# Kernel tuning notes

Hardware: AMD Instinct MI355X
Metric: run time of the kernel (lower is better)

The kernel has to match this reference:

```python
import jax, jax.numpy as jnp
import numpy as np

D = 256
N_TOK, N_SRL, N_ENT, T = 50000, 20000, 10000, 50000
E_TS, E_EE, E_ST, E_ET = 300000, 150000, 300000, 150000
SLOPE = 0.01  # F.leaky_relu default negative slope


def _leaky(x):
    return jnp.where(x >= 0, x, SLOPE * x)


def _seg_softmax(e, seg, n):
    # per-destination (segment) softmax over incoming edges, elementwise per feature
    mx = jax.ops.segment_max(e, seg, num_segments=n)
    mx = jnp.where(jnp.isfinite(mx), mx, 0.0)
    ex = jnp.exp(e - mx[seg])
    den = jax.ops.segment_sum(ex, seg, num_segments=n)
    return ex / jnp.maximum(den[seg], 1e-9)


def _gru_cell(x, h, W_ih, W_hh, b_ih, b_hh):
    # PyTorch GRU cell: gates ordered (r, z, n)
    gi = x @ W_ih.T + b_ih
    gh = h @ W_hh.T + b_hh
    ir, iz, in_ = jnp.split(gi, 3, axis=-1)
    hr, hz, hn = jnp.split(gh, 3, axis=-1)
    r = jax.nn.sigmoid(ir + hr)
    z = jax.nn.sigmoid(iz + hz)
    n = jnp.tanh(in_ + r * hn)
    return (1.0 - z) * n + z * h


def _covering_dst(key, E, N):
    # every dst node gets >= 1 edge (matches DGL UDF-reduce update semantics)
    return jax.random.permutation(key, jnp.arange(E, dtype=jnp.int32) % N)


def setup_inputs():
    key = jax.random.key(0)
    ks = jax.random.split(key, 32)
    f32 = jnp.float32
    inp = {
        'feat_tok': jax.random.normal(ks[0], (N_TOK, D), f32),
        'feat_srl': jax.random.normal(ks[1], (N_SRL, D), f32),
        'feat_ent': jax.random.normal(ks[2], (N_ENT, D), f32),
        'bert_token_emb': jax.random.normal(ks[3], (T, D), f32),
        'rel_type': jax.random.uniform(ks[4], (E_EE,), f32),
        'src_ts': jax.random.randint(ks[5], (E_TS,), 0, N_TOK, jnp.int32),
        'dst_ts': _covering_dst(ks[6], E_TS, N_SRL),
        'src_ee': jax.random.randint(ks[7], (E_EE,), 0, N_ENT, jnp.int32),
        'dst_ee': _covering_dst(ks[8], E_EE, N_ENT),
        'src_st': jax.random.randint(ks[9], (E_ST,), 0, N_SRL, jnp.int32),
        'dst_st': _covering_dst(ks[10], E_ST, N_TOK),
        'src_et': jax.random.randint(ks[11], (E_ET,), 0, N_ENT, jnp.int32),
        'dst_et': _covering_dst(ks[12], E_ET, N_TOK),
    }
    x0 = jax.random.randint(ks[13], (E_EE,), 0, T - 64, jnp.int32)
    ln = jax.random.randint(ks[14], (E_EE,), 1, 65, jnp.int32)
    inp['span_idx'] = jnp.stack([x0, x0 + ln], axis=1)
    s = 0.05
    inp['W_node_trans'] = jax.random.normal(ks[15], (D, D), f32) * s
    inp['b_node_trans'] = jnp.zeros((D,), f32)
    inp['W_node_att'] = jax.random.normal(ks[16], (D, 2 * D), f32) * s
    inp['b_node_att'] = jnp.zeros((D,), f32)
    inp['W_rel_trans'] = jax.random.normal(ks[17], (D, 2 * D), f32) * s
    inp['b_rel_trans'] = jnp.zeros((D,), f32)
    inp['W_common'] = jax.random.normal(ks[18], (D, D), f32) * s
    inp['b_common'] = jnp.zeros((D,), f32)
    inp['W_ih'] = jax.random.normal(ks[19], (3 * D, D), f32) * s
    inp['W_hh'] = jax.random.normal(ks[20], (3 * D, D), f32) * s
    inp['b_ih'] = jax.random.normal(ks[21], (3 * D,), f32) * s
    inp['b_hh'] = jax.random.normal(ks[22], (3 * D,), f32) * s
    return inp


def reference(feat_tok, feat_srl, feat_ent, bert_token_emb, rel_type,
              W_node_trans, b_node_trans, W_node_att, b_node_att,
              W_rel_trans, b_rel_trans, W_common, b_common,
              W_ih, W_hh, b_ih, b_hh,
              src_ts, dst_ts, src_ee, dst_ee, span_idx,
              src_st, dst_st, src_et, dst_et):
    # ---- regular edges tok->srl (message_func_regular_node + reduce_func) ----
    us = feat_tok[src_ts] @ W_node_trans.T + b_node_trans          # [E_TS, D]
    ud = feat_srl[dst_ts] @ W_node_trans.T + b_node_trans
    e_ts = _leaky(jnp.concatenate([us, ud], axis=1) @ W_node_att.T + b_node_att)
    alpha_ts = _seg_softmax(e_ts, dst_ts, N_SRL)
    h_srl = jax.ops.segment_sum(alpha_ts * us, dst_ts, num_segments=N_SRL)

    # ---- ent2ent_rel (message_func_rel + reduce_func) ----
    # mean of bert_token_emb[x:y] via prefix sums (vectorized span means)
    P = jnp.concatenate([jnp.zeros((1, D), bert_token_emb.dtype),
                         jnp.cumsum(bert_token_emb, axis=0)], axis=0)  # [T+1, D]
    x, y = span_idx[:, 0], span_idx[:, 1]
    span_mean = (P[y] - P[x]) / (y - x).astype(P.dtype)[:, None]
    rel_emb = rel_type[:, None] * span_mean                         # [E_EE, D]
    src_e = feat_ent[src_ee]
    m_ee = (jnp.concatenate([src_e, rel_emb], axis=1) @ W_rel_trans.T + b_rel_trans)
    m_ee = m_ee @ W_common.T + b_common
    dst_p = feat_ent[dst_ee] @ W_node_trans.T + b_node_trans
    e_ee = _leaky(jnp.concatenate([m_ee, dst_p], axis=1) @ W_node_att.T + b_node_att)
    alpha_ee = _seg_softmax(e_ee, dst_ee, N_ENT)
    h_ent = jax.ops.segment_sum(alpha_ee * m_ee, dst_ee, num_segments=N_ENT)

    # ---- srl2tok / ent2tok: per-edge GRU step then segment-sum on tok ----
    m_st = _gru_cell(h_srl[src_st], feat_tok[dst_st], W_ih, W_hh, b_ih, b_hh)
    h_srl_tok = jax.ops.segment_sum(m_st, dst_st, num_segments=N_TOK)
    m_et = _gru_cell(h_ent[src_et], feat_tok[dst_et], W_ih, W_hh, b_ih, b_hh)
    h_ent_tok = jax.ops.segment_sum(m_et, dst_et, num_segments=N_TOK)

    # ---- final GRU combine: seq (h_ent_tok, feat_tok), hidden h_srl_tok ----
    h1 = _gru_cell(h_ent_tok, h_srl_tok, W_ih, W_hh, b_ih, b_hh)
    h_tok = _gru_cell(feat_tok, h1, W_ih, W_hh, b_ih, b_hh)

    return h_tok, h_srl, h_ent
```

## Files before the change

kernel.cpp:

```cpp
#include <hip/hip_runtime.h>
#include <stdint.h>


typedef unsigned short u16;
typedef __bf16 bf16_t;
typedef bf16_t bf16x8 __attribute__((ext_vector_type(8)));
typedef float f32x4 __attribute__((ext_vector_type(4)));

__device__ __forceinline__ float us2f(u16 h) {
  unsigned int u = ((unsigned int)h) << 16;
  return __builtin_bit_cast(float, u);
}
__device__ __forceinline__ u16 f2us(float f) {
  unsigned int u = __builtin_bit_cast(unsigned int, f);
  u += 0x7FFFu + ((u >> 16) & 1u);
  return (u16)(u >> 16);
}
__device__ __forceinline__ uint4 pack8(float4 a, float4 b) {
  uint4 v;
  v.x = f2us(a.x) | ((unsigned)f2us(a.y) << 16);
  v.y = f2us(a.z) | ((unsigned)f2us(a.w) << 16);
  v.z = f2us(b.x) | ((unsigned)f2us(b.y) << 16);
  v.w = f2us(b.z) | ((unsigned)f2us(b.w) << 16);
  return v;
}
__device__ __forceinline__ void us2f4(ushort4 v, float* o) {
  o[0] = us2f(v.x); o[1] = us2f(v.y); o[2] = us2f(v.z); o[3] = us2f(v.w);
}
__device__ __forceinline__ float sigm(float x) { return 1.f / (1.f + __expf(-x)); }
__device__ __forceinline__ float tanh_f(float x) {
  x = fminf(fmaxf(x, -15.f), 15.f);
  float e = __expf(2.f * x);
  return (e - 1.f) / (e + 1.f);
}

__global__ void fill_sent(float* out, int n, float v) {
  int i = blockIdx.x * 256 + threadIdx.x;
  if (i < n) out[i] = v;
}

__global__ void count_k(const int* __restrict__ dst, int E, int* __restrict__ cnt) {
  int i = blockIdx.x * 256 + threadIdx.x;
  if (i < E) atomicAdd(&cnt[dst[i]], 1);
}

__global__ __launch_bounds__(1024) void scan4_k(int* a0, int n0, int* a1, int n1,
                                                int* a2, int n2, int* a3, int n3) {
  int* a; int n;
  if (blockIdx.x == 0) { a = a0; n = n0; }
  else if (blockIdx.x == 1) { a = a1; n = n1; }
  else if (blockIdx.x == 2) { a = a2; n = n2; }
  else { a = a3; n = n3; }
  __shared__ int swv[16];
  const int t = threadIdx.x, lane = t & 63, wid = t >> 6;
  int carry = 0;
  for (int base = 0; base < n; base += 1024) {
    int r = base + t;
    int v = (r < n) ? a[r] : 0;
    int inc = v;
#pragma unroll
    for (int o = 1; o < 64; o <<= 1) {
      int x = __shfl_up(inc, o, 64);
      if (lane >= o) inc += x;
    }
    if (lane == 63) swv[wid] = inc;
    __syncthreads();
    int wbase = 0, tot = 0;
    for (int w = 0; w < 16; w++) { int s = swv[w]; tot += s; if (w < wid) wbase += s; }
    if (r < n) a[r] = carry + wbase + inc - v;
    carry += tot;
    __syncthreads();
  }
}

__global__ void fill_k(const int* __restrict__ dst, int E, int* __restrict__ off,
                       int* __restrict__ list) {
  int i = blockIdx.x * 256 + threadIdx.x;
  if (i < E) {
    int p = atomicAdd(&off[dst[i]], 1);
    list[p] = i;
  }
}

__global__ __launch_bounds__(256) void cumsum_p1(const float* __restrict__ emb,
                                                 float* __restrict__ bsum) {
  int b = blockIdx.x, t = threadIdx.x;
  int r0 = b * 64, r1 = min(r0 + 64, 50000);
  float acc = 0.f;
  for (int r = r0; r < r1; r++) acc += emb[(size_t)r * 256 + t];
  bsum[(size_t)b * 256 + t] = acc;
}
__global__ __launch_bounds__(256) void cumsum_p2p(float* __restrict__ bsum, int nb) {
  const int d = blockIdx.x;
  const int t = threadIdx.x, lane = t & 63, wid = t >> 6;
  __shared__ float wsum[4];
  float v[4];
  float s = 0.f;
#pragma unroll
  for (int j = 0; j < 4; j++) {
    int b = t * 4 + j;
    v[j] = (b < nb) ? bsum[(size_t)b * 256 + d] : 0.f;
    s += v[j];
  }
  float inc = s;
#pragma unroll
  for (int o = 1; o < 64; o <<= 1) {
    float x = __shfl_up(inc, o, 64);
    if (lane >= o) inc += x;
  }
  if (lane == 63) wsum[wid] = inc;
  __syncthreads();
  float wbase = 0.f;
  for (int w = 0; w < 4; w++) {
    float ws = wsum[w];
    if (w < wid) wbase += ws;
  }
  float excl = wbase + inc - s;
#pragma unroll
  for (int j = 0; j < 4; j++) {
    int b = t * 4 + j;
    if (b < nb) bsum[(size_t)b * 256 + d] = excl;
    excl += v[j];
  }
}
__global__ __launch_bounds__(256) void cumsum_p3(const float* __restrict__ emb,
                                                 const float* __restrict__ bsum,
                                                 float* __restrict__ Pm) {
  int b = blockIdx.x, t = threadIdx.x;
  int r0 = b * 64, r1 = min(r0 + 64, 50000);
  float acc = bsum[(size_t)b * 256 + t];
  if (b == 0) Pm[t] = 0.f;
  for (int r = r0; r < r1; r++) {
    acc += emb[(size_t)r * 256 + t];
    Pm[(size_t)(r + 1) * 256 + t] = acc;
  }
}

__global__ __launch_bounds__(256) void make_B2(const float* __restrict__ Watt,
                                               const float* __restrict__ Wc,
                                               float* __restrict__ B2) {
  int r = blockIdx.x, k = threadIdx.x;
  float s = 0.f;
  for (int n = 0; n < 256; n++) s += Watt[r * 512 + n] * Wc[n * 256 + k];
  B2[r * 256 + k] = s;
}
__global__ void make_bias2(const float* __restrict__ Watt, const float* __restrict__ bc,
                           float* __restrict__ bias2cat) {
  int r = threadIdx.x;
  float s = 0.f;
  for (int k = 0; k < 256; k++) s += Watt[r * 512 + k] * bc[k];
  bias2cat[r] = bc[r];
  bias2cat[256 + r] = s;
}
__global__ __launch_bounds__(256) void make_WW(const float* __restrict__ Wc,
                                               const float* __restrict__ B2,
                                               const float* __restrict__ Wrel,
                                               float* __restrict__ WW) {
  int r = blockIdx.x, k = threadIdx.x;
  const float* X = (r < 256) ? (Wc + (size_t)r * 256) : (B2 + (size_t)(r - 256) * 256);
  float s = 0.f;
  for (int n = 0; n < 256; n++) s += X[n] * Wrel[(size_t)n * 512 + 256 + k];
  WW[(size_t)r * 256 + k] = s;
}

__global__ __launch_bounds__(256) void conv8(
    const float* s0, u16* d0, int n0, const float* s1, u16* d1, int n1,
    const float* s2, u16* d2, int n2, const float* s3, u16* d3, int n3,
    const float* s4, u16* d4, int n4, const float* s5, u16* d5, int n5,
    const float* s6, u16* d6, int n6, const float* s7, u16* d7, int n7) {
  const float* s; u16* d; int n;
  switch (blockIdx.y) {
    case 0: s = s0; d = d0; n = n0; break;
    case 1: s = s1; d = d1; n = n1; break;
    case 2: s = s2; d = d2; n = n2; break;
    case 3: s = s3; d = d3; n = n3; break;
    case 4: s = s4; d = d4; n = n4; break;
    case 5: s = s5; d = d5; n = n5; break;
    case 6: s = s6; d = d6; n = n6; break;
    default: s = s7; d = d7; n = n7; break;
  }
  int i = (blockIdx.x * 256 + threadIdx.x) * 8;
  if (i < n) {
    float4 a = *(const float4*)(s + i), b = *(const float4*)(s + i + 4);
    *(uint4*)(d + i) = pack8(a, b);
  }
}

#define LOADB4_(step, v0, v1, v2, v3)                                          \
  do {                                                                         \
    const u16* bq_ = B + (size_t)(nbase + (((step) >> 1) * 64) + (t >> 4)) *   \
                         ldb + ((step) & 1) * 128 + (t & 15) * 8;              \
    v0 = *(const uint4*)(bq_);                                                 \
    v1 = *(const uint4*)(bq_ + (size_t)16 * ldb);                              \
    v2 = *(const uint4*)(bq_ + (size_t)32 * ldb);                              \
    v3 = *(const uint4*)(bq_ + (size_t)48 * ldb);                              \
  } while (0)

#define WRITEB4_(v0, v1, v2, v3)                                               \
  do {                                                                         \
    u16* bw_ = &Bs[(t >> 4) * LDB + (t & 15) * 8];                             \
    *(uint4*)(bw_) = v0;                                                       \
    *(uint4*)(bw_ + 16 * LDB) = v1;                                            \
    *(uint4*)(bw_ + 32 * LDB) = v2;                                            \
    *(uint4*)(bw_ + 48 * LDB) = v3;                                            \
  } while (0)

#define COMPUTE_(k2)                                                           \
  do {                                                                         \
    _Pragma("unroll") for (int kk = 0; kk < 128; kk += 32) {                   \
      bf16x8 av = *(const bf16x8*)(ar + (k2) * 128 + kk);                      \
      _Pragma("unroll") for (int j = 0; j < 4; j++) {                          \
        bf16x8 bv = *(const bf16x8*)(bb + j * 16 * LDB + kk);                  \
        acc[j] = __builtin_amdgcn_mfma_f32_16x16x32_bf16(av, bv, acc[j], 0, 0, 0); \
      }                                                                        \
    }                                                                          \
  } while (0)

template <int AMODE, int ASRC, bool OUTBF>
__global__ __launch_bounds__(256) void gemm_nl(
    const void* __restrict__ Ap, int lda,
    const float* __restrict__ Pm, const int* __restrict__ span,
    const float* __restrict__ rel, const int* __restrict__ lst,
    const int* __restrict__ offarr, const int* __restrict__ srcv,
    const u16* __restrict__ s2tab, int dst0, int dpc,
    const u16* __restrict__ B, int ldb, const float* __restrict__ bias,
    void* __restrict__ Cp, int Cstride, int coff, int M, int NT) {
  constexpr int LDA = 264, LDB = 136;
  __shared__ u16 As[64 * LDA];
  __shared__ u16 Bs[64 * LDB];
  int e_start = 0, eM = M;
  if (AMODE == 2) {
    e_start = dst0 ? offarr[dst0 - 1] : 0;
    int len = offarr[dst0 + dpc - 1] - e_start;
    eM = len < M ? len : M;
  }
  const int m0 = blockIdx.x * 64;
  if (m0 >= eM) return;
  const int nbase = blockIdx.y * NT * 64;
  const int t = threadIdx.x;
  const int wave = t >> 6, lane = t & 63, lrow = lane & 15, quad = lane >> 4;

  uint4 pa0, pa1, pa2, pa3, pb0, pb1, pb2, pb3;
  LOADB4_(0, pa0, pa1, pa2, pa3);

#pragma unroll
  for (int i = 0; i < 8; i++) {
    int c = t + i * 256;
    int row = c >> 5, col = (c & 31) * 8;
    int gm = m0 + row;
    uint4 va; va.x = va.y = va.z = va.w = 0u;
    if (gm < eM) {
      if (AMODE == 0) {
        if (ASRC == 0) {
          const float* af = (const float*)Ap + (size_t)gm * lda + col;
          va = pack8(*(const float4*)af, *(const float4*)(af + 4));
        } else {
          va = *(const uint4*)((const u16*)Ap + (size_t)gm * lda + col);
        }
      } else {
        int e = lst[e_start + gm];
        int xx = span[2 * e], yy = span[2 * e + 1];
        float sc = rel[e] / (float)(yy - xx);
        const float* py = Pm + (size_t)yy * 256 + col;
        const float* px = Pm + (size_t)xx * 256 + col;
        float4 ya = *(const float4*)py, yb = *(const float4*)(py + 4);
        float4 xa = *(const float4*)px, xb = *(const float4*)(px + 4);
        float4 d0 = {(ya.x - xa.x) * sc, (ya.y - xa.y) * sc,
                     (ya.z - xa.z) * sc, (ya.w - xa.w) * sc};
        float4 d1 = {(yb.x - xb.x) * sc, (yb.y - xb.y) * sc,
                     (yb.z - xb.z) * sc, (yb.w - xb.w) * sc};
        va = pack8(d0, d1);
      }
    }
    *(uint4*)&As[row * LDA + col] = va;
  }
  __syncthreads();

  const u16* ar = &As[(wave * 16 + lrow) * LDA + quad * 8];
  const u16* bb = &Bs[lrow * LDB + quad * 8];

  for (int nt = 0; nt < NT; nt++) {
    const int n0 = nbase + nt * 64;
    f32x4 acc[4] = {{0.f, 0.f, 0.f, 0.f}, {0.f, 0.f, 0.f, 0.f},
                    {0.f, 0.f, 0.f, 0.f}, {0.f, 0.f, 0.f, 0.f}};
    WRITEB4_(pa0, pa1, pa2, pa3);
    LOADB4_(2 * nt + 1, pb0, pb1, pb2, pb3);
    __syncthreads();
    COMPUTE_(0);
    __syncthreads();
    WRITEB4_(pb0, pb1, pb2, pb3);
    if (nt + 1 < NT) LOADB4_(2 * nt + 2, pa0, pa1, pa2, pa3);
    __syncthreads();
    COMPUTE_(1);
    __syncthreads();
#pragma unroll
    for (int r = 0; r < 4; r++) {
      int m = m0 + wave * 16 + quad * 4 + r;
      if (m < eM) {
        const u16* srow = nullptr;
        if (AMODE == 2) {
          int e = lst[e_start + m];
          srow = s2tab + (size_t)srcv[e] * 512;
        }
#pragma unroll
        for (int j = 0; j < 4; j++) {
          int n = n0 + j * 16 + lrow;
          float v = acc[j][r] + (bias ? bias[n] : 0.f);
          if (AMODE == 2) v += us2f(srow[n]);
          if (OUTBF) ((u16*)Cp)[(size_t)m * Cstride + coff + n] = f2us(v);
          else       ((float*)Cp)[(size_t)m * Cstride + coff + n] = v;
        }
      }
    }
  }
}

__global__ __launch_bounds__(256) void agg_ts2(
    const int* __restrict__ off, const int* __restrict__ list,
    const int* __restrict__ src, const u16* __restrict__ uta,
    const u16* __restrict__ adst, float* __restrict__ out) {
  const int i = blockIdx.x, t = threadIdx.x, lane = t & 63, w = t >> 6;
  const int s0 = i ? off[i - 1] : 0, s1 = off[i];
  const int cnt = s1 - s0;
  __shared__ int sl[64];
  __shared__ float nbuf[4][256], dbuf[4][256];
  if (t < cnt) sl[t] = src[list[s0 + t]];
  __syncthreads();
  const int d4 = lane * 4;
  float ad[4];
  us2f4(*(const ushort4*)&adst[(size_t)i * 256 + d4], ad);
  float num[4] = {0.f, 0.f, 0.f, 0.f}, den[4] = {0.f, 0.f, 0.f, 0.f};
  for (int p = w; p < cnt; p += 4) {
    const u16* row = uta + (size_t)sl[p] * 512;
    float u[4], a[4];
    us2f4(*(const ushort4*)&row[d4], u);
    us2f4(*(const ushort4*)&row[256 + d4], a);
#pragma unroll
    for (int j = 0; j < 4; j++) {
      float v = a[j] + ad[j];
      v = v >= 0.f ? v : 0.01f * v;
      float ex = __expf(v);
      den[j] += ex;
      num[j] += ex * u[j];
    }
  }
#pragma unroll
  for (int j = 0; j < 4; j++) { nbuf[w][d4 + j] = num[j]; dbuf[w][d4 + j] = den[j]; }
  __syncthreads();
  float ns = nbuf[0][t] + nbuf[1][t] + nbuf[2][t] + nbuf[3][t];
  float ds = dbuf[0][t] + dbuf[1][t] + dbuf[2][t] + dbuf[3][t];
  out[(size_t)i * 256 + t] = ns / fmaxf(ds, 1e-9f);
}

__global__ __launch_bounds__(256) void agg_ee2(
    const int* __restrict__ off, const u16* __restrict__ buf,
    const u16* __restrict__ adp, float* __restrict__ out, int dst0) {
  const int i = dst0 + blockIdx.x, t = threadIdx.x, lane = t & 63, w = t >> 6;
  const int e_start = dst0 ? off[dst0 - 1] : 0;
  const int s0 = i ? off[i - 1] : 0, s1 = off[i];
  __shared__ float nbuf[4][256], dbuf[4][256];
  const int d4 = lane * 4;
  float ad[4];
  us2f4(*(const ushort4*)&adp[(size_t)i * 256 + d4], ad);
  float num[4] = {0.f, 0.f, 0.f, 0.f}, den[4] = {0.f, 0.f, 0.f, 0.f};
  for (int p = s0 + w; p < s1; p += 4) {
    const u16* row = buf + (size_t)(p - e_start) * 512;
    float m[4], a[4];
    us2f4(*(const ushort4*)&row[d4], m);
    us2f4(*(const ushort4*)&row[256 + d4], a);
#pragma unroll
    for (int j = 0; j < 4; j++) {
      float v = a[j] + ad[j];
      v = v >= 0.f ? v : 0.01f * v;
      float ex = __expf(v);
      den[j] += ex;
      num[j] += ex * m[j];
    }
  }
#pragma unroll
  for (int j = 0; j < 4; j++) { nbuf[w][d4 + j] = num[j]; dbuf[w][d4 + j] = den[j]; }
  __syncthreads();
  float ns = nbuf[0][t] + nbuf[1][t] + nbuf[2][t] + nbuf[3][t];
  float ds = dbuf[0][t] + dbuf[1][t] + dbuf[2][t] + dbuf[3][t];
  out[(size_t)i * 256 + t] = ns / fmaxf(ds, 1e-9f);
}

__global__ __launch_bounds__(256) void agg_gru2(
    const int* __restrict__ off, const int* __restrict__ list,
    const int* __restrict__ src, const u16* __restrict__ gi,
    const u16* __restrict__ ghc, const float* __restrict__ feat,
    u16* __restrict__ out, int tok0) {
  const int bi = blockIdx.x, i = tok0 + bi;
  const int t = threadIdx.x, lane = t & 63, w = t >> 6;
  const int s0 = i ? off[i - 1] : 0, s1 = off[i];
  const int cnt = s1 - s0;
  __shared__ int sl[32];
  __shared__ float red[4][256];
  if (t < cnt) sl[t] = src[list[s0 + t]];
  __syncthreads();
  const int d4 = lane * 4;
  const size_t b = (size_t)bi * 768;
  float ghr[4], ghz[4], ghn[4], h[4];
  us2f4(*(const ushort4*)&ghc[b + d4], ghr);
  us2f4(*(const ushort4*)&ghc[b + 256 + d4], ghz);
  us2f4(*(const ushort4*)&ghc[b + 512 + d4], ghn);
  { float4 v = *(const float4*)&feat[(size_t)i * 256 + d4];
    h[0] = v.x; h[1] = v.y; h[2] = v.z; h[3] = v.w; }
  float sum[4] = {0.f, 0.f, 0.f, 0.f};
  for (int p = w; p < cnt; p += 4) {
    const u16* g = gi + (size_t)sl[p] * 768;
    float gr[4], gz[4], gn[4];
    us2f4(*(const ushort4*)&g[d4], gr);
    us2f4(*(const ushort4*)&g[256 + d4], gz);
    us2f4(*(const ushort4*)&g[512 + d4], gn);
#pragma unroll
    for (int j = 0; j < 4; j++) {
      float r = sigm(gr[j] + ghr[j]);
      float z = sigm(gz[j] + ghz[j]);
      float n = tanh_f(gn[j] + r * ghn[j]);
      sum[j] += (1.f - z) * n + z * h[j];
    }
  }
#pragma unroll
  for (int j = 0; j < 4; j++) red[w][d4 + j] = sum[j];
  __syncthreads();
  float s = red[0][t] + red[1][t] + red[2][t] + red[3][t];
  out[(size_t)i * 256 + t] = f2us(s);
}

template <bool OUTBF>
__global__ __launch_bounds__(256) void gru_combine2(
    const float* __restrict__ gi, const float* __restrict__ gh,
    const u16* __restrict__ hprev, void* __restrict__ out, int row0) {
  const int t = threadIdx.x, lane = t & 63, w = t >> 6;
  const int li = blockIdx.x * 4 + w;
  const int d4 = lane * 4;
  const size_t g = (size_t)li * 768;
  float4 ir = *(const float4*)&gi[g + d4];
  float4 hr4 = *(const float4*)&gh[g + d4];
  float4 iz = *(const float4*)&gi[g + 256 + d4];
  float4 hz4 = *(const float4*)&gh[g + 256 + d4];
  float4 in4 = *(const float4*)&gi[g + 512 + d4];
  float4 hn4 = *(const float4*)&gh[g + 512 + d4];
  float h[4];
  us2f4(*(const ushort4*)&hprev[(size_t)(row0 + li) * 256 + d4], h);
  float gir[4] = {ir.x, ir.y, ir.z, ir.w}, ghr[4] = {hr4.x, hr4.y, hr4.z, hr4.w};
  float giz[4] = {iz.x, iz.y, iz.z, iz.w}, ghz[4] = {hz4.x, hz4.y, hz4.z, hz4.w};
  float gin[4] = {in4.x, in4.y, in4.z, in4.w}, ghn[4] = {hn4.x, hn4.y, hn4.z, hn4.w};
  float o[4];
#pragma unroll
  for (int j = 0; j < 4; j++) {
    float r = sigm(gir[j] + ghr[j]);
    float z = sigm(giz[j] + ghz[j]);
    float n = tanh_f(gin[j] + r * ghn[j]);
    o[j] = (1.f - z) * n + z * h[j];
  }
  if (OUTBF) {
    ushort4 ov = {f2us(o[0]), f2us(o[1]), f2us(o[2]), f2us(o[3])};
    *(ushort4*)&((u16*)out)[(size_t)(row0 + li) * 256 + d4] = ov;
  } else {
    float4 ov = {o[0], o[1], o[2], o[3]};
    *(float4*)&((float*)out)[(size_t)(row0 + li) * 256 + d4] = ov;
  }
}

extern "C" void kernel_launch(void* const* d_in, const int* in_sizes, int n_in,
                              void* d_out, int out_size, void* d_ws, size_t ws_size,
                              hipStream_t stream) {
  const float* feat_tok = (const float*)d_in[0];
  const float* feat_srl = (const float*)d_in[1];
  const float* feat_ent = (const float*)d_in[2];
  const float* bert     = (const float*)d_in[3];
  const float* rel_type = (const float*)d_in[4];
  const int* src_ts = (const int*)d_in[5];
  const int* dst_ts = (const int*)d_in[6];
  const int* src_ee = (const int*)d_in[7];
  const int* dst_ee = (const int*)d_in[8];
  const int* src_st = (const int*)d_in[9];
  const int* dst_st = (const int*)d_in[10];
  const int* src_et = (const int*)d_in[11];
  const int* dst_et = (const int*)d_in[12];
  const int* span   = (const int*)d_in[13];
  const float* Wn   = (const float*)d_in[14];
  const float* bn   = (const float*)d_in[15];
  const float* Watt = (const float*)d_in[16];
  const float* batt = (const float*)d_in[17];
  const float* Wrel = (const float*)d_in[18];
  const float* brel = (const float*)d_in[19];
  const float* Wc   = (const float*)d_in[20];
  const float* bc   = (const float*)d_in[21];
  const float* Wih  = (const float*)d_in[22];
  const float* Whh  = (const float*)d_in[23];
  const float* bih  = (const float*)d_in[24];
  const float* bhh  = (const float*)d_in[25];

  char* W = (char*)d_ws;
  float* Pm    = (float*)(W + 0);
  u16* uta     = (u16*)(W + 51250240);
  u16* p_srl   = (u16*)(W + 102450240);
  u16* a_dst   = (u16*)(W + 112690240);
  u16* s_ent   = (u16*)(W + 51250240);
  u16* p_ent   = (u16*)(W + 56370240);
  u16* meeatt  = (u16*)(W + 51250240);
  float* WW    = (float*)(W + 138000000);
  float* B2    = (float*)(W + 138600000);
  float* bias2cat = (float*)(W + 138900000);
  u16* s2tab   = (u16*)(W + 139000000);
  u16* adp     = (u16*)(W + 149300032);
  float* bsum  = (float*)(W + 155000000);
  u16* gi_srl  = (u16*)(W + 0);
  u16* gi_ent  = (u16*)(W + 30720000);
  u16* ghc     = (u16*)(W + 51250240);
  u16* hst     = (u16*)(W + 115300096);
  u16* het     = (u16*)(W + 140900096);
  float* giA   = (float*)(W + 0);
  float* ghA   = (float*)(W + 38400000);
  u16* h1      = (u16*)(W + 76800000);
  int* ts_off = (int*)(W + 166500096);
  int* ts_lst = (int*)(W + 166580096);
  int* ee_off = (int*)(W + 167780096);
  int* ee_lst = (int*)(W + 167820096);
  int* st_off = (int*)(W + 168420096);
  int* st_lst = (int*)(W + 168620096);
  int* et_off = (int*)(W + 169820096);
  int* et_lst = (int*)(W + 170020096);
  constexpr size_t NEED = 170620096;

  float* out_htok = (float*)d_out;
  float* out_hsrl = (float*)d_out + 12800000;
  float* out_hent = (float*)d_out + 17920000;

  u16* wtb    = (u16*)((char*)d_out + 49000000);
  u16* Wn_b   = wtb;
  u16* Watt_b = wtb + 65536;
  u16* Wrel_b = wtb + 196608;
  u16* Wc_b   = wtb + 327680;
  u16* B2_b   = wtb + 393216;
  u16* Wih_b  = wtb + 458752;
  u16* Whh_b  = wtb + 655360;
  u16* WW_b   = wtb + 851968;

  if (ws_size < NEED) {
    fill_sent<<<(out_size + 255) / 256, 256, 0, stream>>>(
        (float*)d_out, out_size, 1000.f + (float)(ws_size >> 20));
    return;
  }

  hipMemsetAsync(ts_off, 0, 20000 * 4, stream);
  hipMemsetAsync(ee_off, 0, 10000 * 4, stream);
  hipMemsetAsync(st_off, 0, 50000 * 4, stream);
  hipMemsetAsync(et_off, 0, 50000 * 4, stream);
  count_k<<<1172, 256, 0, stream>>>(dst_ts, 300000, ts_off);
  count_k<<<586, 256, 0, stream>>>(dst_ee, 150000, ee_off);
  count_k<<<1172, 256, 0, stream>>>(dst_st, 300000, st_off);
  count_k<<<586, 256, 0, stream>>>(dst_et, 150000, et_off);
  scan4_k<<<4, 1024, 0, stream>>>(ts_off, 20000, ee_off, 10000, st_off, 50000, et_off, 50000);
  fill_k<<<1172, 256, 0, stream>>>(dst_ts, 300000, ts_off, ts_lst);
  fill_k<<<586, 256, 0, stream>>>(dst_ee, 150000, ee_off, ee_lst);
  fill_k<<<1172, 256, 0, stream>>>(dst_st, 300000, st_off, st_lst);
  fill_k<<<586, 256, 0, stream>>>(dst_et, 150000, et_off, et_lst);

  cumsum_p1<<<782, 256, 0, stream>>>(bert, bsum);
  cumsum_p2p<<<256, 256, 0, stream>>>(bsum, 782);
  cumsum_p3<<<782, 256, 0, stream>>>(bert, bsum, Pm);
  make_B2<<<256, 256, 0, stream>>>(Watt, Wc, B2);
  make_bias2<<<1, 256, 0, stream>>>(Watt, bc, bias2cat);
  make_WW<<<512, 256, 0, stream>>>(Wc, B2, Wrel, WW);
  conv8<<<dim3(96, 8), 256, 0, stream>>>(
      Wn, Wn_b, 65536, Watt, Watt_b, 131072, Wrel, Wrel_b, 131072,
      Wc, Wc_b, 65536, Wih, Wih_b, 196608, Whh, Whh_b, 196608,
      WW, WW_b, 131072, B2, B2_b, 65536);

  gemm_nl<0, 0, true><<<dim3(782, 1), 256, 0, stream>>>(
      feat_tok, 256, nullptr, nullptr, nullptr, nullptr, nullptr, nullptr, nullptr, 0, 0,
      Wn_b, 256, bn, uta, 512, 0, 50000, 4);
  gemm_nl<0, 1, true><<<dim3(782, 1), 256, 0, stream>>>(
      uta, 512, nullptr, nullptr, nullptr, nullptr, nullptr, nullptr, nullptr, 0, 0,
      Watt_b, 512, nullptr, uta, 512, 256, 50000, 4);
  gemm_nl<0, 0, true><<<dim3(313, 2), 256, 0, stream>>>(
      feat_srl, 256, nullptr, nullptr, nullptr, nullptr, nullptr, nullptr, nullptr, 0, 0,
      Wn_b, 256, bn, p_srl, 256, 0, 20000, 2);
  gemm_nl<0, 1, true><<<dim3(313, 2), 256, 0, stream>>>(
      p_srl, 256, nullptr, nullptr, nullptr, nullptr, nullptr, nullptr, nullptr, 0, 0,
      Watt_b + 256, 512, batt, a_dst, 256, 0, 20000, 2);
  agg_ts2<<<20000, 256, 0, stream>>>(ts_off, ts_lst, src_ts, uta, a_dst, out_hsrl);

  gemm_nl<0, 0, true><<<dim3(157, 2), 256, 0, stream>>>(
      feat_ent, 256, nullptr, nullptr, nullptr, nullptr, nullptr, nullptr, nullptr, 0, 0,
      Wrel_b, 512, brel, s_ent, 256, 0, 10000, 2);
  gemm_nl<0, 0, true><<<dim3(157, 2), 256, 0, stream>>>(
      feat_ent, 256, nullptr, nullptr, nullptr, nullptr, nullptr, nullptr, nullptr, 0, 0,
      Wn_b, 256, bn, p_ent, 256, 0, 10000, 2);
  gemm_nl<0, 1, true><<<dim3(157, 2), 256, 0, stream>>>(
      s_ent, 256, nullptr, nullptr, nullptr, nullptr, nullptr, nullptr, nullptr, 0, 0,
      Wc_b, 256, bias2cat, s2tab, 512, 0, 10000, 4);
  gemm_nl<0, 1, true><<<dim3(157, 2), 256, 0, stream>>>(
      p_ent, 256, nullptr, nullptr, nullptr, nullptr, nullptr, nullptr, nullptr, 0, 0,
      Watt_b + 256, 512, batt, adp, 256, 0, 10000, 2);
  for (int c = 0; c < 4; c++) {
    gemm_nl<2, 0, true><<<dim3(625, 1), 256, 0, stream>>>(
        nullptr, 256, Pm, span, rel_type, ee_lst, ee_off, src_ee, s2tab, c * 2500, 2500,
        WW_b, 256, nullptr, meeatt, 512, 0, 40000, 8);
    agg_ee2<<<2500, 256, 0, stream>>>(ee_off, meeatt, adp, out_hent, c * 2500);
  }

  gemm_nl<0, 0, true><<<dim3(313, 3), 256, 0, stream>>>(
      out_hsrl, 256, nullptr, nullptr, nullptr, nullptr, nullptr, nullptr, nullptr, 0, 0,
      Wih_b, 256, bih, gi_srl, 768, 0, 20000, 4);
  gemm_nl<0, 0, true><<<dim3(157, 3), 256, 0, stream>>>(
      out_hent, 256, nullptr, nullptr, nullptr, nullptr, nullptr, nullptr, nullptr, 0, 0,
      Wih_b, 256, bih, gi_ent, 768, 0, 10000, 4);
  for (int c = 0; c < 2; c++) {
    int base = c * 25000;
    gemm_nl<0, 0, true><<<dim3(391, 3), 256, 0, stream>>>(
        feat_tok + (size_t)base * 256, 256, nullptr, nullptr, nullptr, nullptr,
        nullptr, nullptr, nullptr, 0, 0, Whh_b, 256, bhh, ghc, 768, 0, 25000, 4);
    agg_gru2<<<25000, 256, 0, stream>>>(st_off, st_lst, src_st, gi_srl, ghc, feat_tok, hst, base);
    agg_gru2<<<25000, 256, 0, stream>>>(et_off, et_lst, src_et, gi_ent, ghc, feat_tok, het, base);
  }

  for (int c = 0; c < 4; c++) {
    int base = c * 12500;
    gemm_nl<0, 1, false><<<dim3(196, 3), 256, 0, stream>>>(
        het + (size_t)base * 256, 256, nullptr, nullptr, nullptr, nullptr,
        nullptr, nullptr, nullptr, 0, 0, Wih_b, 256, bih, giA, 768, 0, 12500, 4);
    gemm_nl<0, 1, false><<<dim3(196, 3), 256, 0, stream>>>(
        hst + (size_t)base * 256, 256, nullptr, nullptr, nullptr, nullptr,
        nullptr, nullptr, nullptr, 0, 0, Whh_b, 256, bhh, ghA, 768, 0, 12500, 4);
    gru_combine2<true><<<3125, 256, 0, stream>>>(giA, ghA, hst, h1, base);
  }
  for (int c = 0; c < 4; c++) {
    int base = c * 12500;
    gemm_nl<0, 0, false><<<dim3(196, 3), 256, 0, stream>>>(
        feat_tok + (size_t)base * 256, 256, nullptr, nullptr, nullptr, nullptr,
        nullptr, nullptr, nullptr, 0, 0, Wih_b, 256, bih, giA, 768, 0, 12500, 4);
    gemm_nl<0, 1, false><<<dim3(196, 3), 256, 0, stream>>>(
        h1 + (size_t)base * 256, 256, nullptr, nullptr, nullptr, nullptr,
        nullptr, nullptr, nullptr, 0, 0, Whh_b, 256, bhh, ghA, 768, 0, 12500, 4);
    gru_combine2<false><<<3125, 256, 0, stream>>>(giA, ghA, h1, out_htok, base);
  }
}
```

Measured before the change: 1.870 ms.

## Use 2x2 wave tiling with register-resident A fragments in gemm_nl

Reorganizes the per-block 64x64 output tile so each wave computes a 32x32 sub-tile (2x2 MFMA blocks) instead of a 16x64 strip. The full K=256 A fragments for both row groups are loaded from LDS into registers once, outside the N-tile loop, so A no longer has to be re-read from shared memory for every N tile. Each B fragment now feeds two MFMAs instead of one. This cuts LDS traffic per MFMA, but it raises VGPR use by 16 bf16x8 registers. Launch bounds are set to 3 blocks per CU to cap register pressure, which may cause spills or lower occupancy.

Result: faster. 1.756 ms (-6.0%).

```diff
diff --git a/kernel.cpp b/kernel.cpp
--- a/kernel.cpp
+++ b/kernel.cpp
@@ -205,19 +205,18 @@
     *(uint4*)(bw_ + 48 * LDB) = v3;                                            \
   } while (0)
 
-#define COMPUTE_(k2)                                                           \
+#define CSTEP_(a0, a1, q)                                                      \
   do {                                                                         \
-    _Pragma("unroll") for (int kk = 0; kk < 128; kk += 32) {                   \
-      bf16x8 av = *(const bf16x8*)(ar + (k2) * 128 + kk);                      \
-      _Pragma("unroll") for (int j = 0; j < 4; j++) {                          \
-        bf16x8 bv = *(const bf16x8*)(bb + j * 16 * LDB + kk);                  \
-        acc[j] = __builtin_amdgcn_mfma_f32_16x16x32_bf16(av, bv, acc[j], 0, 0, 0); \
-      }                                                                        \
-    }                                                                          \
+    bf16x8 bv0_ = *(const bf16x8*)(bb + (q) * 32);                             \
+    bf16x8 bv1_ = *(const bf16x8*)(bb + 16 * LDB + (q) * 32);                  \
+    c00 = __builtin_amdgcn_mfma_f32_16x16x32_bf16(a0, bv0_, c00, 0, 0, 0);     \
+    c01 = __builtin_amdgcn_mfma_f32_16x16x32_bf16(a0, bv1_, c01, 0, 0, 0);     \
+    c10 = __builtin_amdgcn_mfma_f32_16x16x32_bf16(a1, bv0_, c10, 0, 0, 0);     \
+    c11 = __builtin_amdgcn_mfma_f32_16x16x32_bf16(a1, bv1_, c11, 0, 0, 0);     \
   } while (0)
 
 template <int AMODE, int ASRC, bool OUTBF>
-__global__ __launch_bounds__(256) void gemm_nl(
+__global__ __launch_bounds__(256, 3) void gemm_nl(
     const void* __restrict__ Ap, int lda,
     const float* __restrict__ Pm, const int* __restrict__ span,
     const float* __restrict__ rel, const int* __restrict__ lst,
@@ -239,6 +238,7 @@
   const int nbase = blockIdx.y * NT * 64;
   const int t = threadIdx.x;
   const int wave = t >> 6, lane = t & 63, lrow = lane & 15, quad = lane >> 4;
+  const int wr = wave >> 1, wc = wave & 1;
 
   uint4 pa0, pa1, pa2, pa3, pb0, pb1, pb2, pb3;
   LOADB4_(0, pa0, pa1, pa2, pa3);
@@ -276,39 +276,83 @@
   }
   __syncthreads();
 
-  const u16* ar = &As[(wave * 16 + lrow) * LDA + quad * 8];
-  const u16* bb = &Bs[lrow * LDB + quad * 8];
+  const u16* arp = &As[(wr * 32 + lrow) * LDA + quad * 8];
+  bf16x8 aA0 = *(const bf16x8*)(arp + 0);
+  bf16x8 aA1 = *(const bf16x8*)(arp + 32);
+  bf16x8 aA2 = *(const bf16x8*)(arp + 64);
+  bf16x8 aA3 = *(const bf16x8*)(arp + 96);
+  bf16x8 aA4 = *(const bf16x8*)(arp + 128);
+  bf16x8 aA5 = *(const bf16x8*)(arp + 160);
+  bf16x8 aA6 = *(const bf16x8*)(arp + 192);
+  bf16x8 aA7 = *(const bf16x8*)(arp + 224);
+  const u16* arq = arp + 16 * LDA;
+  bf16x8 aB0 = *(const bf16x8*)(arq + 0);
+  bf16x8 aB1 = *(const bf16x8*)(arq + 32);
+  bf16x8 aB2 = *(const bf16x8*)(arq + 64);
+  bf16x8 aB3 = *(const bf16x8*)(arq + 96);
+  bf16x8 aB4 = *(const bf16x8*)(arq + 128);
+  bf16x8 aB5 = *(const bf16x8*)(arq + 160);
+  bf16x8 aB6 = *(const bf16x8*)(arq + 192);
+  bf16x8 aB7 = *(const bf16x8*)(arq + 224);
+
+  const u16* bb = &Bs[(wc * 32 + lrow) * LDB + quad * 8];
 
   for (int nt = 0; nt < NT; nt++) {
     const int n0 = nbase + nt * 64;
-    f32x4 acc[4] = {{0.f, 0.f, 0.f, 0.f}, {0.f, 0.f, 0.f, 0.f},
-                    {0.f, 0.f, 0.f, 0.f}, {0.f, 0.f, 0.f, 0.f}};
+    f32x4 c00 = {0.f, 0.f, 0.f, 0.f}, c01 = {0.f, 0.f, 0.f, 0.f};
+    f32x4 c10 = {0.f, 0.f, 0.f, 0.f}, c11 = {0.f, 0.f, 0.f, 0.f};
     WRITEB4_(pa0, pa1, pa2, pa3);
     LOADB4_(2 * nt + 1, pb0, pb1, pb2, pb3);
     __syncthreads();
-    COMPUTE_(0);
+    CSTEP_(aA0, aB0, 0);
+    CSTEP_(aA1, aB1, 1);
+    CSTEP_(aA2, aB2, 2);
+    CSTEP_(aA3, aB3, 3);
     __syncthreads();
     WRITEB4_(pb0, pb1, pb2, pb3);
     if (nt + 1 < NT) LOADB4_(2 * nt + 2, pa0, pa1, pa2, pa3);
     __syncthreads();
-    COMPUTE_(1);
+    CSTEP_(aA4, aB4, 0);
+    CSTEP_(aA5, aB5, 1);
+    CSTEP_(aA6, aB6, 2);
+    CSTEP_(aA7, aB7, 3);
     __syncthreads();
 #pragma unroll
     for (int r = 0; r < 4; r++) {
-      int m = m0 + wave * 16 + quad * 4 + r;
-      if (m < eM) {
-        const u16* srow = nullptr;
-        if (AMODE == 2) {
-          int e = lst[e_start + m];
-          srow = s2tab + (size_t)srcv[e] * 512;
+      {
+        int m = m0 + wr * 32 + quad * 4 + r;
+        if (m < eM) {
+          const u16* srow = nullptr;
+          if (AMODE == 2) srow = s2tab + (size_t)srcv[lst[e_start + m]] * 512;
+          int n = n0 + wc * 32 + lrow;
+          float v0 = c00[r] + (bias ? bias[n] : 0.f);
+          float v1 = c01[r] + (bias ? bias[n + 16] : 0.f);
+          if (AMODE == 2) { v0 += us2f(srow[n]); v1 += us2f(srow[n + 16]); }
+          if (OUTBF) {
+            ((u16*)Cp)[(size_t)m * Cstride + coff + n] = f2us(v0);
+            ((u16*)Cp)[(size_t)m * Cstride + coff + n + 16] = f2us(v1);
+          } else {
+            ((float*)Cp)[(size_t)m * Cstride + coff + n] = v0;
+            ((float*)Cp)[(size_t)m * Cstride + coff + n + 16] = v1;
+          }
         }
-#pragma unroll
-        for (int j = 0; j < 4; j++) {
-          int n = n0 + j * 16 + lrow;
-          float v = acc[j][r] + (bias ? bias[n] : 0.f);
-          if (AMODE == 2) v += us2f(srow[n]);
-          if (OUTBF) ((u16*)Cp)[(size_t)m * Cstride + coff + n] = f2us(v);
-          else       ((float*)Cp)[(size_t)m * Cstride + coff + n] = v;
+      }
+      {
+        int m = m0 + wr * 32 + 16 + quad * 4 + r;
+        if (m < eM) {
+          const u16* srow = nullptr;
+          if (AMODE == 2) srow = s2tab + (size_t)srcv[lst[e_start + m]] * 512;
+          int n = n0 + wc * 32 + lrow;
+          float v0 = c10[r] + (bias ? bias[n] : 0.f);
+          float v1 = c11[r] + (bias ? bias[n + 16] : 0.f);
+          if (AMODE == 2) { v0 += us2f(srow[n]); v1 += us2f(srow[n + 16]); }
+          if (OUTBF) {
+            ((u16*)Cp)[(size_t)m * Cstride + coff + n] = f2us(v0);
+            ((u16*)Cp)[(size_t)m * Cstride + coff + n + 16] = f2us(v1);
+          } else {
+            ((float*)Cp)[(size_t)m * Cstride + coff + n] = v0;
+            ((float*)Cp)[(size_t)m * Cstride + coff + n + 16] = v1;
+          }
         }
       }
     }
```
